# Optimization experiments

Measured on AMD Instinct MI355X. Metric: run time of the kernel, lower is better.

## Reference

```python
import jax, jax.numpy as jnp
import numpy as np

BS, C, H, W = 16, 64, 128, 128
NC = 80          # num classes (hardcoded 80 in original via expand(-1, 80, -1))
TOPK = 128
TAU = 0.07
EPS = 1e-12      # F.normalize eps


def setup_inputs() -> dict:
    key = jax.random.key(0)
    k1, k2, k3, k4 = jax.random.split(key, 4)
    feat = jax.random.normal(k1, (BS, C, H, W), dtype=jnp.float32)
    score = jax.random.uniform(k2, (BS, NC, H, W), dtype=jnp.float32)
    # hm: GT heatmap with exactly one 1.0 peak per (batch, class) for ~half the classes
    pos = jax.random.randint(k3, (BS, NC), 0, H * W)
    present = jax.random.bernoulli(k4, 0.5, (BS, NC)).astype(jnp.float32)
    b = jnp.arange(BS)[:, None]
    c = jnp.arange(NC)[None, :]
    hm = jnp.zeros((BS, NC, H * W), jnp.float32).at[b, c, pos].set(present)
    hm = hm.reshape(BS, NC, H, W)
    return {"feat": feat, "score": score, "hm": hm}


def reference(feat, score, hm):
    bs, c, h, w = feat.shape
    nc = hm.shape[1]
    hw = h * w
    score = jax.lax.stop_gradient(score)  # score.detach()

    # F.normalize(feat, dim=1)
    feat = feat / jnp.maximum(jnp.linalg.norm(feat, axis=1, keepdims=True), EPS)

    # q: feature at the hm==1 peak of each present class (one peak per (b,cls))
    peak = (hm == 1.0).astype(feat.dtype)                       # [bs,nc,h,w]
    q = jnp.einsum('bnhw,bchw->bnc', peak, feat)                # [bs,nc,c]
    class_mask = (peak.sum(axis=(2, 3)) > 0).astype(feat.dtype)  # [bs,nc]

    # k0: hm-weighted pooled feature per class, L2-normalized
    k0 = jnp.einsum('bchw,bnhw->bnc', feat, hm)                 # [bs,nc,c]
    k0 = k0 / jnp.maximum(jnp.linalg.norm(k0, axis=-1, keepdims=True), EPS)

    # mask score: zero at GT locations and for absent classes
    hm_free = (hm.sum(axis=1) == 0).astype(score.dtype)         # [bs,h,w]
    score = score * hm_free[:, None] * class_mask[:, :, None, None]

    max_values = score.max(axis=1).reshape(bs, hw)              # [bs,hw]
    class_indices = score.argmax(axis=1).reshape(bs, hw)        # [bs,hw]
    topk_values, topk_indices = jax.lax.top_k(max_values, TOPK)  # [bs,topk]
    k_all_mask_t = (topk_values > 0).astype(feat.dtype)         # [bs,topk]
    topk_class = jnp.take_along_axis(class_indices, topk_indices, axis=1)  # [bs,topk]

    feat_flat = feat.reshape(bs, c, hw)
    k_top = jnp.take_along_axis(feat_flat, topk_indices[:, None, :], axis=2)  # [bs,c,topk]
    k_top = k_top.transpose(0, 2, 1)                            # [bs,topk,c]

    # pseudo heatmap: 0.9 at selected (class, pos) pairs with positive score
    b_idx = jnp.arange(bs)[:, None]
    pseudo_hm = jnp.zeros((bs, nc, hw), feat.dtype).at[
        b_idx, topk_class, topk_indices].set(k_all_mask_t * 0.9)
    pseudo_hm = pseudo_hm.reshape(bs, nc, h, w)

    # positive mask: selected positions whose pseudo class matches the query class
    class_ids = jnp.arange(nc, dtype=feat.dtype)
    target = jnp.where(class_mask[:, :, None] == 1, class_ids[None, :, None], -1.0)  # [bs,nc,1]
    k_mask_top = (target == topk_class[:, None, :].astype(feat.dtype)).astype(feat.dtype)
    k_mask_top = k_mask_top * k_all_mask_t[:, None, :]          # [bs,nc,topk]
    k0_mask = class_mask[:, :, None] * jnp.eye(nc, dtype=feat.dtype)  # [bs,nc,nc]

    k_all = jnp.concatenate([k_top, k0], axis=1)                # [bs,topk+nc,c]
    k_mask = jnp.concatenate([k_mask_top, k0_mask], axis=-1)    # [bs,nc,topk+nc]
    k_all_mask = jnp.concatenate([k_all_mask_t, class_mask], axis=-1)  # [bs,topk+nc]

    sim = jnp.exp(jnp.einsum('bnc,bkc->bnk', q, k_all) / TAU)   # [bs,nc,topk+nc]
    sim_sum = (sim * k_all_mask[:, None, :]).sum(-1, keepdims=True)
    sim_sum = jnp.where(sim_sum == 0, 1.0, sim_sum)
    logit = jnp.where(k_mask > 0, sim / sim_sum, 1.0)
    log_loss = (jnp.log(logit) * k_mask).sum(-1)                # [bs,nc]
    num = k_mask.sum(-1)
    num = jnp.where(num == 0, 1.0, num)
    count = class_mask.sum()
    loss = ((log_loss / num) * class_mask).sum() / count
    return (-loss, pseudo_hm)
```

## Files before the change

kernel.cpp:

```cpp
#include <hip/hip_runtime.h>
#include <math.h>

#define BS 16
#define C 64
#define H 128
#define W 128
#define HW (H*W)
#define NC 80
#define TOPK 128
#define KALL (TOPK+NC)
#define TAU 0.07f
#define EPSN 1e-12f
#define OUT_N 20971521
#define NCHW (NC*HW)
#define WBLK 2560

__global__ __launch_bounds__(1024) void k_peak(const float* __restrict__ hm,
                                               int* __restrict__ peak_pos) {
    __shared__ int wmax[16];
    int bn = blockIdx.x, t = threadIdx.x;
    int lane = t & 63, wid = t >> 6;
    const float4* p = (const float4*)(hm + (size_t)bn * HW);
    int found = -1;
    #pragma unroll
    for (int j = 0; j < 4; ++j) {
        int gi = j * 1024 + t;
        float4 v = p[gi];
        int base = gi * 4;
        if (v.x == 1.0f) found = base;
        if (v.y == 1.0f) found = base + 1;
        if (v.z == 1.0f) found = base + 2;
        if (v.w == 1.0f) found = base + 3;
    }
    #pragma unroll
    for (int off = 1; off < 64; off <<= 1) found = max(found, __shfl_xor(found, off));
    if (lane == 0) wmax[wid] = found;
    __syncthreads();
    if (t == 0) {
        int m = wmax[0];
        #pragma unroll
        for (int i = 1; i < 16; ++i) m = max(m, wmax[i]);
        peak_pos[bn] = m;
    }
}

__global__ void k_max(const float* __restrict__ score, const int* __restrict__ peak_pos,
                      float* __restrict__ maxv, int* __restrict__ clsidx) {
    __shared__ int pk[NC];
    int b = blockIdx.y;
    int g = blockIdx.x * blockDim.x + threadIdx.x;
    if (threadIdx.x < NC) pk[threadIdx.x] = peak_pos[b * NC + threadIdx.x];
    __syncthreads();
    const float4* sb = (const float4*)(score + (size_t)b * NC * HW);
    int p0 = g * 4;
    int pp0 = pk[0];
    float m0 = (pp0 >= 0) ? 1.0f : 0.0f;
    float4 v0 = sb[g];
    float bx = v0.x * m0, by = v0.y * m0, bz = v0.z * m0, bw = v0.w * m0;
    int ix = 0, iy = 0, iz = 0, iw = 0;
    bool pe0 = (pp0 == p0), pe1 = (pp0 == p0 + 1), pe2 = (pp0 == p0 + 2), pe3 = (pp0 == p0 + 3);
    #pragma unroll 8
    for (int n = 1; n < NC; ++n) {
        int pp = pk[n];
        float m = (pp >= 0) ? 1.0f : 0.0f;
        float4 v = sb[(size_t)n * (HW / 4) + g];
        float vx = v.x * m, vy = v.y * m, vz = v.z * m, vw = v.w * m;
        if (vx > bx) { bx = vx; ix = n; }
        if (vy > by) { by = vy; iy = n; }
        if (vz > bz) { bz = vz; iz = n; }
        if (vw > bw) { bw = vw; iw = n; }
        pe0 |= (pp == p0); pe1 |= (pp == p0 + 1); pe2 |= (pp == p0 + 2); pe3 |= (pp == p0 + 3);
    }
    if (pe0) { bx = 0.0f; ix = 0; }
    if (pe1) { by = 0.0f; iy = 0; }
    if (pe2) { bz = 0.0f; iz = 0; }
    if (pe3) { bw = 0.0f; iw = 0; }
    ((float4*)maxv)[(size_t)b * (HW / 4) + g] = make_float4(bx, by, bz, bw);
    ((int4*)clsidx)[(size_t)b * (HW / 4) + g] = make_int4(ix, iy, iz, iw);
}

__global__ __launch_bounds__(1024) void k_topk(const float* __restrict__ maxv,
                                               const int* __restrict__ clsidx,
                                               float* __restrict__ topkv,
                                               int* __restrict__ topki,
                                               int* __restrict__ topkc,
                                               unsigned char* __restrict__ map) {
    __shared__ unsigned int hist[2048];
    __shared__ unsigned int wtot[16];
    __shared__ unsigned int woff[16];
    __shared__ unsigned int s_pref;
    __shared__ int s_rank;
    __shared__ unsigned int s_bin;
    __shared__ unsigned int s_above;

    int b = blockIdx.x, t = threadIdx.x;
    int lane = t & 63, wid = t >> 6;

    {
        unsigned int* mz = (unsigned int*)(map + (size_t)b * HW);
        #pragma unroll
        for (int j = 0; j < 4; ++j) mz[j * 1024 + t] = 0u;
    }

    unsigned int key[16];
    const float4* mv4 = (const float4*)(maxv + (size_t)b * HW);
    #pragma unroll
    for (int j4 = 0; j4 < 4; ++j4) {
        float4 v = mv4[t * 4 + j4];
        key[j4 * 4 + 0] = __float_as_uint(v.x);
        key[j4 * 4 + 1] = __float_as_uint(v.y);
        key[j4 * 4 + 2] = __float_as_uint(v.z);
        key[j4 * 4 + 3] = __float_as_uint(v.w);
    }

    if (t == 0) { s_pref = 0u; s_rank = TOPK; }

    const int shifts[3] = {21, 10, 0};
    const int widths[3] = {11, 11, 10};

    for (int rnd = 0; rnd < 3; ++rnd) {
        int sh = shifts[rnd], w = widths[rnd];
        unsigned mask = (1u << w) - 1u;
        hist[t] = 0u; hist[t + 1024] = 0u;
        __syncthreads();
        unsigned pref = s_pref;
        int hiShift = sh + w;
        #pragma unroll
        for (int j = 0; j < 16; ++j) {
            unsigned k = key[j];
            bool ok = (rnd == 0) || ((k >> hiShift) == pref);
            if (ok) atomicAdd(&hist[(k >> sh) & mask], 1u);
        }
        __syncthreads();
        unsigned p = hist[2 * t] + hist[2 * t + 1];
        unsigned s = p;
        #pragma unroll
        for (int off = 1; off < 64; off <<= 1) {
            unsigned o = __shfl_down(s, off);
            if (lane + off < 64) s += o;
        }
        if (lane == 0) wtot[wid] = s;
        __syncthreads();
        if (wid == 0) {
            unsigned vv = (lane < 16) ? wtot[lane] : 0u;
            unsigned ss = vv;
            #pragma unroll
            for (int off = 1; off < 64; off <<= 1) {
                unsigned o = __shfl_down(ss, off);
                if (lane + off < 64) ss += o;
            }
            if (lane < 16) woff[lane] = ss - vv;
        }
        __syncthreads();
        unsigned S_t = s + woff[wid];
        unsigned S_next = S_t - p;
        int r = s_rank;
        if ((int)S_t >= r && (int)S_next < r) {
            unsigned hi = hist[2 * t + 1];
            if ((int)(S_next + hi) >= r) { s_bin = 2u * t + 1u; s_above = S_next; }
            else                         { s_bin = 2u * t;      s_above = S_next + hi; }
        }
        __syncthreads();
        if (t == 0) {
            s_pref = (s_pref << w) | s_bin;
            s_rank = s_rank - (int)s_above;
        }
        __syncthreads();
    }
    unsigned K = s_pref;
    int need_eq = s_rank;
    int cnt_gt = TOPK - need_eq;

    int cg = 0, ce = 0;
    #pragma unroll
    for (int j = 0; j < 16; ++j) { cg += (key[j] > K); ce += (key[j] == K); }
    unsigned v = ((unsigned)cg << 16) | (unsigned)ce;
    unsigned sc = v;
    #pragma unroll
    for (int off = 1; off < 64; off <<= 1) {
        unsigned o = __shfl_up(sc, off);
        if (lane >= off) sc += o;
    }
    if (lane == 63) wtot[wid] = sc;
    __syncthreads();
    if (wid == 0) {
        unsigned vv = (lane < 16) ? wtot[lane] : 0u;
        unsigned ss = vv;
        #pragma unroll
        for (int off = 1; off < 64; off <<= 1) {
            unsigned o = __shfl_up(ss, off);
            if (lane >= off) ss += o;
        }
        if (lane < 16) woff[lane] = ss - vv;
    }
    __syncthreads();
    unsigned ex = (sc - v) + woff[wid];
    int pg = (int)(ex >> 16);
    int pe = (int)(ex & 0xffffu);
    int lg = 0, le = 0;
    #pragma unroll
    for (int j = 0; j < 16; ++j) {
        unsigned k = key[j];
        int slot = -1;
        if (k > K) { slot = pg + lg; ++lg; }
        else if (k == K) { int er = pe + le; ++le; if (er < need_eq) slot = cnt_gt + er; }
        if (slot >= 0) {
            int idx = t * 16 + j;
            int cls = clsidx[(size_t)b * HW + idx];
            topkv[b * TOPK + slot] = __uint_as_float(k);
            topki[b * TOPK + slot] = idx;
            topkc[b * TOPK + slot] = cls;
            if (__uint_as_float(k) > 0.0f)
                map[(size_t)b * HW + idx] = (unsigned char)(cls + 1);
        }
    }
}

__global__ void k_gather(const float* __restrict__ feat, const int* __restrict__ peak_pos,
                         const int* __restrict__ topki, float* k_all, float* qv) {
    int bk = blockIdx.x;
    int b = bk / KALL, k = bk % KALL, c = threadIdx.x;
    int pos;
    if (k < TOPK) {
        pos = topki[b * TOPK + k];
    } else {
        int n = k - TOPK;
        int pp = peak_pos[b * NC + n];
        if (pp < 0) {
            k_all[((size_t)b * KALL + k) * C + c] = 0.0f;
            qv[((size_t)b * NC + n) * C + c] = 0.0f;
            return;
        }
        pos = pp;
    }
    float v = feat[((size_t)b * C + c) * HW + pos];
    float ss = v * v;
    #pragma unroll
    for (int off = 1; off < 64; off <<= 1) ss += __shfl_xor(ss, off);
    float qc = v / fmaxf(sqrtf(ss), EPSN);
    if (k < TOPK) {
        k_all[((size_t)b * KALL + k) * C + c] = qc;
    } else {
        int n = k - TOPK;
        qv[((size_t)b * NC + n) * C + c] = qc;
        float qq = qc * qc;
        #pragma unroll
        for (int off = 1; off < 64; off <<= 1) qq += __shfl_xor(qq, off);
        k_all[((size_t)b * KALL + k) * C + c] = qc / fmaxf(sqrtf(qq), EPSN);
    }
}

__global__ __launch_bounds__(256) void k_loss(const float* __restrict__ k_all,
                                              const float* __restrict__ qv,
                                              const int* __restrict__ peak_pos,
                                              const float* __restrict__ topkv,
                                              const int* __restrict__ topkc,
                                              float* __restrict__ loss_bn) {
    __shared__ float qs[C];
    __shared__ float r1[256];
    __shared__ float r2[256];
    __shared__ float s_simsum, s_num;
    int bn = blockIdx.x;
    int b = bn / NC, n = bn % NC, t = threadIdx.x;
    if (peak_pos[bn] < 0) { if (t == 0) loss_bn[bn] = 0.0f; return; }
    if (t < C) qs[t] = qv[(size_t)bn * C + t];
    __syncthreads();
    float sim = 0.0f, kam = 0.0f, km = 0.0f;
    if (t < KALL) {
        const float* kr = k_all + ((size_t)b * KALL + t) * C;
        float dot = 0.0f;
        for (int c2 = 0; c2 < C; ++c2) dot += qs[c2] * kr[c2];
        sim = expf(dot / TAU);
        if (t < TOPK) {
            float posm = (topkv[b * TOPK + t] > 0.0f) ? 1.0f : 0.0f;
            kam = posm;
            km = (topkc[b * TOPK + t] == n) ? posm : 0.0f;
        } else {
            int j = t - TOPK;
            kam = (peak_pos[b * NC + j] >= 0) ? 1.0f : 0.0f;
            km = (j == n) ? 1.0f : 0.0f;
        }
    }
    r1[t] = sim * kam;
    r2[t] = km;
    __syncthreads();
    for (int s = 128; s > 0; s >>= 1) {
        if (t < s) { r1[t] += r1[t + s]; r2[t] += r2[t + s]; }
        __syncthreads();
    }
    if (t == 0) {
        float ss = r1[0];
        s_simsum = (ss == 0.0f) ? 1.0f : ss;
        s_num = (r2[0] == 0.0f) ? 1.0f : r2[0];
    }
    __syncthreads();
    r1[t] = (km > 0.0f) ? logf(sim / s_simsum) : 0.0f;
    __syncthreads();
    for (int s = 128; s > 0; s >>= 1) {
        if (t < s) r1[t] += r1[t + s];
        __syncthreads();
    }
    if (t == 0) loss_bn[bn] = r1[0] / s_num;
}

__global__ __launch_bounds__(256) void k_write_final(const unsigned char* __restrict__ map,
                                                     const float* __restrict__ loss_bn,
                                                     const int* __restrict__ peak_pos,
                                                     float* __restrict__ out) {
    int t = threadIdx.x;
    if (blockIdx.x < WBLK) {
        int base = blockIdx.x * 8192 + t;
        #pragma unroll
        for (int k = 0; k < 32; ++k) {
            int linear = base + k * 256;
            int hi = linear >> 14;
            int bb = hi / NC;
            int n1 = hi - bb * NC + 1;
            int pos = linear & (HW - 1);
            unsigned char mp = map[(bb << 14) + pos];
            float v = (mp == (unsigned char)n1) ? 0.9f : 0.0f;
            __builtin_nontemporal_store(v, &out[1 + linear]);
        }
        return;
    }
    __shared__ float r1[256];
    __shared__ float r2[256];
    float s = 0.0f, cnt = 0.0f;
    for (int i = t; i < BS * NC; i += 256) {
        s += loss_bn[i];
        cnt += (peak_pos[i] >= 0) ? 1.0f : 0.0f;
    }
    r1[t] = s; r2[t] = cnt;
    __syncthreads();
    for (int st = 128; st > 0; st >>= 1) {
        if (t < st) { r1[t] += r1[t + st]; r2[t] += r2[t + st]; }
        __syncthreads();
    }
    if (t == 0) out[0] = -(r1[0] / r2[0]);
}

extern "C" void kernel_launch(void* const* d_in, const int* in_sizes, int n_in,
                              void* d_out, int out_size, void* d_ws, size_t ws_size,
                              hipStream_t stream) {
    const float* feat  = (const float*)d_in[0];
    const float* score = (const float*)d_in[1];
    const float* hm    = (const float*)d_in[2];
    float* out = (float*)d_out;

    char* ws = (char*)d_ws;
    size_t off = 0;
    auto alloc = [&](size_t bytes) -> void* {
        void* p = ws + off;
        off += (bytes + 255) & ~(size_t)255;
        return p;
    };
    int*   peak_pos = (int*)  alloc((size_t)BS * NC * 4);
    float* maxv     = (float*)alloc((size_t)BS * HW * 4);
    int*   clsidx   = (int*)  alloc((size_t)BS * HW * 4);
    float* topkv    = (float*)alloc((size_t)BS * TOPK * 4);
    int*   topki    = (int*)  alloc((size_t)BS * TOPK * 4);
    int*   topkc    = (int*)  alloc((size_t)BS * TOPK * 4);
    float* k_all    = (float*)alloc((size_t)BS * KALL * C * 4);
    float* qv       = (float*)alloc((size_t)BS * NC * C * 4);
    float* loss_bn  = (float*)alloc((size_t)BS * NC * 4);
    unsigned char* map = (unsigned char*)alloc((size_t)BS * HW);

    k_peak<<<BS * NC, 1024, 0, stream>>>(hm, peak_pos);
    dim3 gmax(HW / 4 / 256, BS);
    k_max<<<gmax, 256, 0, stream>>>(score, peak_pos, maxv, clsidx);
    k_topk<<<BS, 1024, 0, stream>>>(maxv, clsidx, topkv, topki, topkc, map);
    k_gather<<<BS * KALL, 64, 0, stream>>>(feat, peak_pos, topki, k_all, qv);
    k_loss<<<BS * NC, 256, 0, stream>>>(k_all, qv, peak_pos, topkv, topkc, loss_bn);
    k_write_final<<<WBLK + 1, 256, 0, stream>>>(map, loss_bn, peak_pos, out);
}
```

Before: 101.8 us.

## Fuse pseudo-heatmap write into gather kernel with float4 stores

Moves the large pseudo_hm output write out of the final kernel and into the gather kernel, so the 80MB store stream runs alongside the feature gather and ahead of the loss kernel. The write now uses 16-byte float4 stores aligned by shifting the index by one, with a few boundary elements handled by a single thread. The gather is repacked to four 64-lane waves per 256-thread block, and the last kernel becomes a single-block loss reduction. The change drops the nontemporal store hint and adds scalar edge-case handling.

```diff
diff --git a/kernel.cpp b/kernel.cpp
--- a/kernel.cpp
+++ b/kernel.cpp
@@ -14,6 +14,7 @@
 #define OUT_N 20971521
 #define NCHW (NC*HW)
 #define WBLK 2560
+#define GBLK (BS*KALL/4)
 
 __global__ __launch_bounds__(1024) void k_peak(const float* __restrict__ hm,
                                                int* __restrict__ peak_pos) {
@@ -216,10 +217,53 @@
     }
 }
 
-__global__ void k_gather(const float* __restrict__ feat, const int* __restrict__ peak_pos,
-                         const int* __restrict__ topki, float* k_all, float* qv) {
-    int bk = blockIdx.x;
-    int b = bk / KALL, k = bk % KALL, c = threadIdx.x;
+__global__ __launch_bounds__(256) void k_write_gather(const unsigned char* __restrict__ map,
+                                                      const float* __restrict__ feat,
+                                                      const int* __restrict__ peak_pos,
+                                                      const int* __restrict__ topki,
+                                                      float* __restrict__ k_all,
+                                                      float* __restrict__ qv,
+                                                      float* __restrict__ out) {
+    int t = threadIdx.x;
+    if (blockIdx.x < WBLK) {
+        float4* o4 = (float4*)out;
+        #pragma unroll
+        for (int j = 0; j < 8; ++j) {
+            int g = blockIdx.x * 2048 + j * 256 + t;
+            if (g == 0) continue;
+            float r[4];
+            #pragma unroll
+            for (int e = 0; e < 4; ++e) {
+                int linear = 4 * g - 1 + e;
+                int hi = linear >> 14;
+                int bb = hi / NC;
+                int n1 = hi - bb * NC + 1;
+                int pos = linear & (HW - 1);
+                unsigned char mp = map[(bb << 14) + pos];
+                r[e] = (mp == (unsigned char)n1) ? 0.9f : 0.0f;
+            }
+            o4[g] = make_float4(r[0], r[1], r[2], r[3]);
+        }
+        if (blockIdx.x == 0 && t == 0) {
+            #pragma unroll
+            for (int e = 0; e < 3; ++e) {
+                int linear = e;
+                unsigned char mp = map[linear & (HW - 1)];
+                out[1 + linear] = (mp == (unsigned char)1) ? 0.9f : 0.0f;
+            }
+            int linear = OUT_N - 2;
+            int hi = linear >> 14;
+            int bb = hi / NC;
+            int n1 = hi - bb * NC + 1;
+            int pos = linear & (HW - 1);
+            unsigned char mp = map[(bb << 14) + pos];
+            out[OUT_N - 1] = (mp == (unsigned char)n1) ? 0.9f : 0.0f;
+        }
+        return;
+    }
+    int wid = t >> 6, lane = t & 63;
+    int bk = (blockIdx.x - WBLK) * 4 + wid;
+    int b = bk / KALL, k = bk % KALL, c = lane;
     int pos;
     if (k < TOPK) {
         pos = topki[b * TOPK + k];
@@ -303,28 +347,12 @@
     if (t == 0) loss_bn[bn] = r1[0] / s_num;
 }
 
-__global__ __launch_bounds__(256) void k_write_final(const unsigned char* __restrict__ map,
-                                                     const float* __restrict__ loss_bn,
-                                                     const int* __restrict__ peak_pos,
-                                                     float* __restrict__ out) {
-    int t = threadIdx.x;
-    if (blockIdx.x < WBLK) {
-        int base = blockIdx.x * 8192 + t;
-        #pragma unroll
-        for (int k = 0; k < 32; ++k) {
-            int linear = base + k * 256;
-            int hi = linear >> 14;
-            int bb = hi / NC;
-            int n1 = hi - bb * NC + 1;
-            int pos = linear & (HW - 1);
-            unsigned char mp = map[(bb << 14) + pos];
-            float v = (mp == (unsigned char)n1) ? 0.9f : 0.0f;
-            __builtin_nontemporal_store(v, &out[1 + linear]);
-        }
-        return;
-    }
+__global__ __launch_bounds__(256) void k_final(const float* __restrict__ loss_bn,
+                                               const int* __restrict__ peak_pos,
+                                               float* __restrict__ out) {
     __shared__ float r1[256];
     __shared__ float r2[256];
+    int t = threadIdx.x;
     float s = 0.0f, cnt = 0.0f;
     for (int i = t; i < BS * NC; i += 256) {
         s += loss_bn[i];
@@ -369,7 +397,8 @@
     dim3 gmax(HW / 4 / 256, BS);
     k_max<<<gmax, 256, 0, stream>>>(score, peak_pos, maxv, clsidx);
     k_topk<<<BS, 1024, 0, stream>>>(maxv, clsidx, topkv, topki, topkc, map);
-    k_gather<<<BS * KALL, 64, 0, stream>>>(feat, peak_pos, topki, k_all, qv);
+    k_write_gather<<<WBLK + GBLK, 256, 0, stream>>>(map, feat, peak_pos, topki,
+                                                    k_all, qv, out);
     k_loss<<<BS * NC, 256, 0, stream>>>(k_all, qv, peak_pos, topkv, topkc, loss_bn);
-    k_write_final<<<WBLK + 1, 256, 0, stream>>>(map, loss_bn, peak_pos, out);
-}
+    k_final<<<1, 256, 0, stream>>>(loss_bn, peak_pos, out);
+}
```

Result: faster. 98.86 us (-2.9%).
